# Performance work log

Hardware: AMD Instinct MI355X
Metric: run time of the kernel (lower is better)

## Reference

```python
import jax, jax.numpy as jnp
import numpy as np

T, H, W = 4, 16, 16
S = T * H * W          # 1024 flattened sequence length
C = 576                # embd_dim
NH = 8                 # n_head
DK = C // NH           # 72 per-head dim
L = 4                  # n_layer
B = 4                  # batch
PD = C // 3            # 192 per-axis pos-embed dim


def setup_inputs() -> dict:
    key = jax.random.key(0)
    ks = jax.random.split(key, 10)
    s = 1.0 / np.sqrt(C)
    return {
        "x": jax.random.normal(ks[0], (B, T, H, W, C), jnp.float32),
        "pos0": jax.random.normal(ks[1], (T, PD), jnp.float32) * 0.01,
        "pos1": jax.random.normal(ks[2], (H, PD), jnp.float32) * 0.01,
        "pos2": jax.random.normal(ks[3], (W, PD), jnp.float32) * 0.01,
        "ln1_g": jnp.ones((L, C), jnp.float32),
        "ln1_b": jnp.zeros((L, C), jnp.float32),
        "wq": jax.random.normal(ks[4], (L, C, C), jnp.float32) * s,
        "wk": jax.random.normal(ks[5], (L, C, C), jnp.float32) * s,
        "wv": jax.random.normal(ks[6], (L, C, C), jnp.float32) * s,
        "wo": jax.random.normal(ks[7], (L, C, C), jnp.float32) * (s / np.sqrt(L)),
        "wo_b": jnp.zeros((L, C), jnp.float32),
        "ln2_g": jnp.ones((L, C), jnp.float32),
        "ln2_b": jnp.zeros((L, C), jnp.float32),
        "w1": jax.random.normal(ks[8], (L, C, 4 * C), jnp.float32) * s,
        "b1": jnp.zeros((L, 4 * C), jnp.float32),
        "w2": jax.random.normal(ks[9], (L, 4 * C, C), jnp.float32) * (s / 2.0),
        "b2": jnp.zeros((L, C), jnp.float32),
    }


def _layernorm(x, g, b):
    # Faithful to the source: float32 math, and (1e-5 + rsqrt(var)) multiplier
    # (note: source adds eps to rsqrt, not to var -- replicated exactly).
    xf = x.astype(jnp.float32)
    mu = xf.mean(-1, keepdims=True)
    var = jnp.mean(jnp.square(xf - mu), -1, keepdims=True)
    y = (xf - mu) * (1e-5 + jax.lax.rsqrt(var)) * g + b
    return y.astype(x.dtype)


def _stack(x, pos0, pos1, pos2, ln1_g, ln1_b, wq, wk, wv, wo, wo_b,
           ln2_g, ln2_b, w1, b1, w2, b2):
    b = x.shape[0]
    xf = x.reshape(b, S, C)
    # right_shift (decode_step=None): shift flattened tokens right by one
    xf = jnp.pad(xf[:, :-1], ((0, 0), (1, 0), (0, 0)))
    # broadcast positional embedding, concat along channel
    pos = jnp.concatenate([
        jnp.broadcast_to(pos0[:, None, None, :], (T, H, W, PD)),
        jnp.broadcast_to(pos1[None, :, None, :], (T, H, W, PD)),
        jnp.broadcast_to(pos2[None, None, :, :], (T, H, W, PD)),
    ], axis=-1).reshape(S, C)
    xf = xf + pos

    causal = jnp.tril(jnp.ones((S, S), bool))
    scale = 1.0 / np.sqrt(DK)
    neg_inf = jnp.float32(-jnp.inf)

    for l in range(L):  # fixed small layer loop
        # --- causal full self-attention ---
        h = _layernorm(xf, ln1_g[l], ln1_b[l])
        q = (h @ wq[l]).reshape(b, S, NH, DK).transpose(0, 2, 1, 3)
        k = (h @ wk[l]).reshape(b, S, NH, DK).transpose(0, 2, 1, 3)
        v = (h @ wv[l]).reshape(b, S, NH, DK).transpose(0, 2, 1, 3)
        att = jnp.einsum('bhqd,bhkd->bhqk', q, k) * scale
        att = jnp.where(causal, att, neg_inf)
        att = jax.nn.softmax(att, axis=-1)
        a = jnp.einsum('bhqk,bhkd->bhqd', att, v)
        a = a.transpose(0, 2, 1, 3).reshape(b, S, C)
        xf = xf + a @ wo[l] + wo_b[l]
        # --- FFN with GeLU2: sigmoid(1.702*x)*x ---
        h = _layernorm(xf, ln2_g[l], ln2_b[l])
        h = h @ w1[l] + b1[l]
        h = jax.nn.sigmoid(1.702 * h) * h
        xf = xf + h @ w2[l] + b2[l]
    return xf.reshape(b, T, H, W, C)


def reference(x, pos0, pos1, pos2, ln1_g, ln1_b, wq, wk, wv, wo, wo_b,
              ln2_g, ln2_b, w1, b1, w2, b2):
    return _stack(x, pos0, pos1, pos2, ln1_g, ln1_b, wq, wk, wv, wo, wo_b,
                  ln2_g, ln2_b, w1, b1, w2, b2)
```

## Files before the change

kernel.cpp:

```cpp
#include <hip/hip_runtime.h>
#include <hip/hip_bf16.h>

typedef __hip_bfloat16 bf16;
using bf16x8 = __attribute__((ext_vector_type(8))) short;
using f32x4  = __attribute__((ext_vector_type(4))) float;

#define S_LEN 1024
#define CDIM  576
#define NHEAD 8
#define DKH   72
#define BATCH 4
#define MROWS 4096
#define FFDIM 2304
#define QKVN  1728

__device__ __forceinline__ void gload16(const void* g, void* l) {
  __builtin_amdgcn_global_load_lds(
      (const __attribute__((address_space(1))) unsigned int*)g,
      (__attribute__((address_space(3))) unsigned int*)l, 16, 0, 0);
}

template <int N> __device__ __forceinline__ void wait_vmcnt() {
  if constexpr (N == 0)      asm volatile("s_waitcnt vmcnt(0)" ::: "memory");
  else if constexpr (N == 2) asm volatile("s_waitcnt vmcnt(2)" ::: "memory");
  else if constexpr (N == 3) asm volatile("s_waitcnt vmcnt(3)" ::: "memory");
  else if constexpr (N == 4) asm volatile("s_waitcnt vmcnt(4)" ::: "memory");
  else if constexpr (N == 6) asm volatile("s_waitcnt vmcnt(6)" ::: "memory");
}

__device__ __forceinline__ short f2bf_bits(float x) {
  unsigned int u = __float_as_uint(x);
  u += 0x7fffu + ((u >> 16) & 1u);
  return (short)(u >> 16);
}

__global__ __launch_bounds__(256) void transpose_cvt(
    const float* __restrict__ in, bf16* __restrict__ out, int K, int N,
    size_t in_ls, size_t out_ls) {
  __shared__ float tile[32][33];
  const float* inl = in + (size_t)blockIdx.z * in_ls;
  bf16* outl = out + (size_t)blockIdx.z * out_ls;
  int n0 = blockIdx.x * 32, k0 = blockIdx.y * 32;
  int tx = threadIdx.x & 31, ty = threadIdx.x >> 5;
#pragma unroll
  for (int i = 0; i < 32; i += 8)
    tile[ty + i][tx] = inl[(size_t)(k0 + ty + i) * N + (n0 + tx)];
  __syncthreads();
#pragma unroll
  for (int i = 0; i < 32; i += 8)
    outl[(size_t)(n0 + ty + i) * K + (k0 + tx)] = __float2bfloat16(tile[tx][ty + i]);
}

__global__ __launch_bounds__(256) void build_xf(
    const float* __restrict__ x, const float* __restrict__ p0,
    const float* __restrict__ p1, const float* __restrict__ p2,
    float* __restrict__ xf) {
  int idx = blockIdx.x * 256 + threadIdx.x;
  int c4 = idx % 144;
  int s  = (idx / 144) & (S_LEN - 1);
  int b  = idx / (144 * S_LEN);
  int c  = c4 * 4;
  int t = s >> 8, hh = (s >> 4) & 15, w = s & 15;
  float4 pv;
  if (c < 192)       pv = *(const float4*)&p0[t  * 192 + c];
  else if (c < 384)  pv = *(const float4*)&p1[hh * 192 + c - 192];
  else               pv = *(const float4*)&p2[w  * 192 + c - 384];
  float4 xv = make_float4(0.f, 0.f, 0.f, 0.f);
  if (s > 0) xv = *(const float4*)&x[((size_t)b * S_LEN + s - 1) * CDIM + c];
  float4 r = make_float4(xv.x + pv.x, xv.y + pv.y, xv.z + pv.z, xv.w + pv.w);
  *(float4*)&xf[((size_t)b * S_LEN + s) * CDIM + c] = r;
}

__global__ __launch_bounds__(256) void ln_kernel(
    const float* __restrict__ x, const float* __restrict__ g,
    const float* __restrict__ b, bf16* __restrict__ out) {
  int row  = blockIdx.x * 4 + (threadIdx.x >> 6);
  int lane = threadIdx.x & 63;
  const float* xr = x + (size_t)row * CDIM;
  float vals[9];
  float sum = 0.f;
#pragma unroll
  for (int i = 0; i < 9; i++) { vals[i] = xr[lane + 64 * i]; sum += vals[i]; }
#pragma unroll
  for (int o = 1; o < 64; o <<= 1) sum += __shfl_xor(sum, o);
  float mu = sum * (1.f / CDIM);
  float vs = 0.f;
#pragma unroll
  for (int i = 0; i < 9; i++) { float d = vals[i] - mu; vs += d * d; }
#pragma unroll
  for (int o = 1; o < 64; o <<= 1) vs += __shfl_xor(vs, o);
  float mult = 1e-5f + rsqrtf(vs * (1.f / CDIM));
  bf16* orow = out + (size_t)row * CDIM;
#pragma unroll
  for (int i = 0; i < 9; i++) {
    int c = lane + 64 * i;
    orow[c] = __float2bfloat16((vals[i] - mu) * mult * g[c] + b[c]);
  }
}

template <int BM, int BN, bool BIAS, bool RES, int ACT, bool OUTBF>
__global__ __launch_bounds__(256) void gemm3(
    const bf16* __restrict__ A, const bf16* __restrict__ Bt,
    const float* __restrict__ bias, const float* __restrict__ res,
    void* __restrict__ outp, int N, int K) {
  constexpr int MI = BM / 32;
  constexpr int NI = BN / 32;
  constexpr int AJ = BM / 64;
  constexpr int BJ = BN / 64;
  constexpr int LPS = AJ + BJ;
  __shared__ __align__(16) short ldsA[4][BM * 32];
  __shared__ __align__(16) short ldsB[4][BN * 32];
  const int tid = threadIdx.x, lane = tid & 63, wave = tid >> 6;
  const int lr = lane & 15, quad = lane >> 4;
  const int m0 = blockIdx.x * BM, n0 = blockIdx.y * BN;
  const int wm = (wave & 1) * (BM / 2), wn = (wave >> 1) * (BN / 2);
  f32x4 acc[MI][NI] = {};

  const int srow = lane >> 2, scol = (lane & 3) * 8;
  const short* Ag[AJ];
  int ldsAo[AJ];
#pragma unroll
  for (int j = 0; j < AJ; j++) {
    Ag[j] = (const short*)A + (size_t)(m0 + (wave * AJ + j) * 16 + srow) * K + scol;
    ldsAo[j] = (wave * AJ + j) * 512;
  }
  const short* Bg[BJ];
  int ldsBo[BJ];
#pragma unroll
  for (int j = 0; j < BJ; j++) {
    Bg[j] = (const short*)Bt + (size_t)(n0 + (wave * BJ + j) * 16 + srow) * K + scol;
    ldsBo[j] = (wave * BJ + j) * 512;
  }

#pragma unroll
  for (int j = 0; j < AJ; j++) gload16(Ag[j], &ldsA[0][ldsAo[j]]);
#pragma unroll
  for (int j = 0; j < BJ; j++) gload16(Bg[j], &ldsB[0][ldsBo[j]]);
#pragma unroll
  for (int j = 0; j < AJ; j++) gload16(Ag[j] + 32, &ldsA[1][ldsAo[j]]);
#pragma unroll
  for (int j = 0; j < BJ; j++) gload16(Bg[j] + 32, &ldsB[1][ldsBo[j]]);

  int bi = 0;
  for (int k0 = 0; k0 < K; k0 += 32, bi = (bi + 1) & 3) {
    if (k0 + 64 < K) {
      const int sb = (bi + 2) & 3;
#pragma unroll
      for (int j = 0; j < AJ; j++) gload16(Ag[j] + k0 + 64, &ldsA[sb][ldsAo[j]]);
#pragma unroll
      for (int j = 0; j < BJ; j++) gload16(Bg[j] + k0 + 64, &ldsB[sb][ldsBo[j]]);
      wait_vmcnt<2 * LPS>();
    } else if (k0 + 32 < K) {
      wait_vmcnt<LPS>();
    } else {
      wait_vmcnt<0>();
    }
    __builtin_amdgcn_s_barrier();
    __builtin_amdgcn_sched_barrier(0);
    bf16x8 af[MI], bfv[NI];
#pragma unroll
    for (int mi = 0; mi < MI; mi++)
      af[mi] = *(const bf16x8*)&ldsA[bi][(wm + mi * 16 + lr) * 32 + quad * 8];
#pragma unroll
    for (int ni = 0; ni < NI; ni++)
      bfv[ni] = *(const bf16x8*)&ldsB[bi][(wn + ni * 16 + lr) * 32 + quad * 8];
#pragma unroll
    for (int mi = 0; mi < MI; mi++)
#pragma unroll
      for (int ni = 0; ni < NI; ni++)
        acc[mi][ni] = __builtin_amdgcn_mfma_f32_16x16x32_bf16(af[mi], bfv[ni], acc[mi][ni], 0, 0, 0);
  }

  float* fout = (float*)outp;
  bf16*  bout = (bf16*)outp;
#pragma unroll
  for (int mi = 0; mi < MI; mi++)
#pragma unroll
    for (int ni = 0; ni < NI; ni++) {
      int col = n0 + wn + ni * 16 + lr;
#pragma unroll
      for (int r = 0; r < 4; r++) {
        int row = m0 + wm + mi * 16 + quad * 4 + r;
        float v = acc[mi][ni][r];
        if (BIAS) v += bias[col];
        if (ACT == 1) v = v / (1.f + __expf(-1.702f * v));
        size_t idx = (size_t)row * N + col;
        if (RES) v += res[idx];
        if (OUTBF) bout[idx] = __float2bfloat16(v);
        else       fout[idx] = v;
      }
    }
}

__global__ __launch_bounds__(256) void attn_mfma(
    const bf16* __restrict__ qkv, bf16* __restrict__ a) {
  __shared__ __align__(16) short ldsK[2][9 * 512];
  __shared__ __align__(16) short ldsVt[2][80][104];
  __shared__ __align__(16) short ldsP[4 * 1024];
  const int bh = blockIdx.y, b = bh >> 3, h = bh & 7;
  const int tid = threadIdx.x, wave = tid >> 6, lane = tid & 63;
  const int lr = lane & 15, quad = lane >> 4;
  const int qt = (blockIdx.y < 16) ? (15 - (int)blockIdx.x) : (int)blockIdx.x;
  const float scale = 0.11785113019775793f;
  const int qcol = h * DKH, kcol = CDIM + h * DKH, vcol = 2 * CDIM + h * DKH;

  const int qrow = qt * 64 + wave * 16 + lr;
  const short* qg = (const short*)qkv + (size_t)(b * S_LEN + qrow) * QKVN + qcol;
  bf16x8 qfrag[3];
#pragma unroll
  for (int c = 0; c < 3; c++) {
    int d0 = c * 32 + quad * 8;
    bf16x8 z = {0, 0, 0, 0, 0, 0, 0, 0};
    qfrag[c] = (d0 < DKH) ? *(const bf16x8*)(qg + d0) : z;
  }
  f32x4 oacc[5] = {};
  float m[4], l[4];
#pragma unroll
  for (int r = 0; r < 4; r++) { m[r] = -1e30f; l[r] = 0.f; }

  const size_t ktstep = (size_t)64 * QKVN;
  const short* kg0 = (const short*)qkv + (size_t)(b * S_LEN + wave * 16 + lr) * QKVN + kcol + quad * 8;
  const short* kg2 = (const short*)qkv + (size_t)(b * S_LEN + lane) * QKVN + kcol + 64;
  const int vkey = tid & 63, vdgb = tid >> 6;
  const short* vg0 = (const short*)qkv + (size_t)(b * S_LEN + vkey) * QKVN + vcol;

  {
#pragma unroll
    for (int c = 0; c < 2; c++)
      gload16(kg0 + c * 32, &ldsK[0][(wave * 2 + c) * 512]);
    if (wave == 0) gload16(kg2, &ldsK[0][8 * 512]);
#pragma unroll
    for (int pass = 0; pass < 3; pass++) {
      int d0 = (vdgb + pass * 4) * 8;
      if (d0 < 80) {
        bf16x8 vv = {0, 0, 0, 0, 0, 0, 0, 0};
        if (d0 < DKH) vv = *(const bf16x8*)(vg0 + d0);
#pragma unroll
        for (int j = 0; j < 8; j++) ldsVt[0][d0 + j][vkey] = vv[j];
      }
    }
  }
  __syncthreads();

  for (int kt = 0; kt <= qt; kt++) {
    const int cur = kt & 1, nxt = cur ^ 1;
    const bool pf = (kt < qt);
    bf16x8 vpre[3];
    if (pf) {
      const short* kg = kg0 + (size_t)(kt + 1) * ktstep;
#pragma unroll
      for (int c = 0; c < 2; c++)
        gload16(kg + c * 32, &ldsK[nxt][(wave * 2 + c) * 512]);
      if (wave == 0) gload16(kg2 + (size_t)(kt + 1) * ktstep, &ldsK[nxt][8 * 512]);
      const short* vg = vg0 + (size_t)(kt + 1) * ktstep;
#pragma unroll
      for (int pass = 0; pass < 3; pass++) {
        int d0 = (vdgb + pass * 4) * 8;
        bf16x8 z = {0, 0, 0, 0, 0, 0, 0, 0};
        vpre[pass] = (d0 < DKH) ? *(const bf16x8*)(vg + d0) : z;
      }
    }
    f32x4 sacc[4] = {};
    __builtin_amdgcn_s_setprio(1);
#pragma unroll
    for (int nc = 0; nc < 4; nc++) {
      bf16x8 kf0 = *(const bf16x8*)&ldsK[cur][(nc * 2 + 0) * 512 + lane * 8];
      sacc[nc] = __builtin_amdgcn_mfma_f32_16x16x32_bf16(qfrag[0], kf0, sacc[nc], 0, 0, 0);
      bf16x8 kf1 = *(const bf16x8*)&ldsK[cur][(nc * 2 + 1) * 512 + lane * 8];
      sacc[nc] = __builtin_amdgcn_mfma_f32_16x16x32_bf16(qfrag[1], kf1, sacc[nc], 0, 0, 0);
      bf16x8 kf2 = *(const bf16x8*)&ldsK[cur][8 * 512 + (nc * 16 + lr) * 8];
      sacc[nc] = __builtin_amdgcn_mfma_f32_16x16x32_bf16(qfrag[2], kf2, sacc[nc], 0, 0, 0);
    }
    __builtin_amdgcn_s_setprio(0);
    float pmax[4];
#pragma unroll
    for (int r = 0; r < 4; r++) pmax[r] = -1e30f;
    bool diag = (kt == qt);
#pragma unroll
    for (int nc = 0; nc < 4; nc++)
#pragma unroll
      for (int r = 0; r < 4; r++) {
        float s = sacc[nc][r] * scale;
        if (diag && (nc * 16 + lr > wave * 16 + quad * 4 + r)) s = -1e30f;
        sacc[nc][r] = s;
        pmax[r] = fmaxf(pmax[r], s);
      }
    bool within = (pmax[0] - m[0] <= 8.f) && (pmax[1] - m[1] <= 8.f) &&
                  (pmax[2] - m[2] <= 8.f) && (pmax[3] - m[3] <= 8.f);
    if (!__all(within)) {
      float tmax[4];
#pragma unroll
      for (int r = 0; r < 4; r++) {
        tmax[r] = pmax[r];
        tmax[r] = fmaxf(tmax[r], __shfl_xor(tmax[r], 1));
        tmax[r] = fmaxf(tmax[r], __shfl_xor(tmax[r], 2));
        tmax[r] = fmaxf(tmax[r], __shfl_xor(tmax[r], 4));
        tmax[r] = fmaxf(tmax[r], __shfl_xor(tmax[r], 8));
      }
#pragma unroll
      for (int r = 0; r < 4; r++) {
        float mn = fmaxf(m[r], tmax[r]);
        float alpha = __expf(m[r] - mn);
        m[r] = mn;
        l[r] *= alpha;
#pragma unroll
        for (int dc = 0; dc < 5; dc++) oacc[dc][r] *= alpha;
      }
    }
    float psum[4];
#pragma unroll
    for (int r = 0; r < 4; r++) psum[r] = 0.f;
#pragma unroll
    for (int nc = 0; nc < 4; nc++)
#pragma unroll
      for (int r = 0; r < 4; r++) {
        float p = __expf(sacc[nc][r] - m[r]);
        psum[r] += p;
        int col = nc * 16 + lr;
        ldsP[wave * 1024 + (col >> 5) * 512 +
             (((col >> 3) & 3) * 16 + quad * 4 + r) * 8 + (col & 7)] = f2bf_bits(p);
      }
    bf16x8 pfrag[2];
#pragma unroll
    for (int kc = 0; kc < 2; kc++)
      pfrag[kc] = *(const bf16x8*)&ldsP[wave * 1024 + kc * 512 + lane * 8];
    __builtin_amdgcn_s_setprio(1);
#pragma unroll
    for (int dc = 0; dc < 5; dc++)
#pragma unroll
      for (int kc = 0; kc < 2; kc++) {
        bf16x8 vf = *(const bf16x8*)&ldsVt[cur][dc * 16 + lr][kc * 32 + quad * 8];
        oacc[dc] = __builtin_amdgcn_mfma_f32_16x16x32_bf16(pfrag[kc], vf, oacc[dc], 0, 0, 0);
      }
    __builtin_amdgcn_s_setprio(0);
#pragma unroll
    for (int r = 0; r < 4; r++) {
      psum[r] += __shfl_xor(psum[r], 1);
      psum[r] += __shfl_xor(psum[r], 2);
      psum[r] += __shfl_xor(psum[r], 4);
      psum[r] += __shfl_xor(psum[r], 8);
      l[r] += psum[r];
    }
    if (pf) {
#pragma unroll
      for (int pass = 0; pass < 3; pass++) {
        int d0 = (vdgb + pass * 4) * 8;
        if (d0 < 80) {
#pragma unroll
          for (int j = 0; j < 8; j++) ldsVt[nxt][d0 + j][vkey] = vpre[pass][j];
        }
      }
    }
    __syncthreads();
  }

#pragma unroll
  for (int dc = 0; dc < 5; dc++) {
    int d = dc * 16 + lr;
    if (d < DKH) {
#pragma unroll
      for (int r = 0; r < 4; r++) {
        int row = qt * 64 + wave * 16 + quad * 4 + r;
        float val = oacc[dc][r] / l[r];
        a[(size_t)(b * S_LEN + row) * CDIM + h * DKH + d] = __float2bfloat16(val);
      }
    }
  }
}

extern "C" void kernel_launch(void* const* d_in, const int* in_sizes, int n_in,
                              void* d_out, int out_size, void* d_ws, size_t ws_size,
                              hipStream_t stream) {
  const float* x    = (const float*)d_in[0];
  const float* pos0 = (const float*)d_in[1];
  const float* pos1 = (const float*)d_in[2];
  const float* pos2 = (const float*)d_in[3];
  const float* ln1g = (const float*)d_in[4];
  const float* ln1b = (const float*)d_in[5];
  const float* wq   = (const float*)d_in[6];
  const float* wk   = (const float*)d_in[7];
  const float* wv   = (const float*)d_in[8];
  const float* wo   = (const float*)d_in[9];
  const float* wob  = (const float*)d_in[10];
  const float* ln2g = (const float*)d_in[11];
  const float* ln2b = (const float*)d_in[12];
  const float* w1   = (const float*)d_in[13];
  const float* b1   = (const float*)d_in[14];
  const float* w2   = (const float*)d_in[15];
  const float* b2   = (const float*)d_in[16];

  char* ws = (char*)d_ws;
  size_t off = 0;
  auto alloc = [&](size_t bytes) {
    char* p = ws + off;
    off += (bytes + 255) & ~(size_t)255;
    return p;
  };
  bf16* wqkvT = (bf16*)alloc((size_t)4 * QKVN * CDIM * sizeof(bf16));
  bf16* woT   = (bf16*)alloc((size_t)4 * CDIM * CDIM * sizeof(bf16));
  bf16* w1T   = (bf16*)alloc((size_t)4 * FFDIM * CDIM * sizeof(bf16));
  bf16* w2T   = (bf16*)alloc((size_t)4 * CDIM * FFDIM * sizeof(bf16));
  bf16* hbuf  = (bf16*)alloc((size_t)MROWS * CDIM * sizeof(bf16));
  bf16* abuf  = (bf16*)alloc((size_t)MROWS * CDIM * sizeof(bf16));
  bf16* ubuf  = (bf16*)alloc((size_t)MROWS * FFDIM * sizeof(bf16));
  bf16* qkvb  = (bf16*)alloc((size_t)MROWS * QKVN * sizeof(bf16));
  float* xf   = (float*)d_out;

  const size_t ils  = (size_t)CDIM * CDIM;
  const size_t ils2 = (size_t)CDIM * FFDIM;
  const size_t qkv_ls = (size_t)QKVN * CDIM;
  transpose_cvt<<<dim3(18, 18, 4), 256, 0, stream>>>(wq, wqkvT, CDIM, CDIM, ils, qkv_ls);
  transpose_cvt<<<dim3(18, 18, 4), 256, 0, stream>>>(wk, wqkvT + (size_t)CDIM * CDIM, CDIM, CDIM, ils, qkv_ls);
  transpose_cvt<<<dim3(18, 18, 4), 256, 0, stream>>>(wv, wqkvT + (size_t)2 * CDIM * CDIM, CDIM, CDIM, ils, qkv_ls);
  transpose_cvt<<<dim3(18, 18, 4), 256, 0, stream>>>(wo, woT, CDIM, CDIM, ils, ils);
  transpose_cvt<<<dim3(72, 18, 4), 256, 0, stream>>>(w1, w1T, CDIM, FFDIM, ils2, ils2);
  transpose_cvt<<<dim3(18, 72, 4), 256, 0, stream>>>(w2, w2T, FFDIM, CDIM, ils2, ils2);

  build_xf<<<2304, 256, 0, stream>>>(x, pos0, pos1, pos2, xf);

  for (int l = 0; l < 4; l++) {
    bf16* wqkv_l = wqkvT + (size_t)l * qkv_ls;
    bf16* wo_l   = woT   + (size_t)l * ils;
    bf16* w1_l   = w1T   + (size_t)l * ils2;
    bf16* w2_l   = w2T   + (size_t)l * ils2;

    ln_kernel<<<1024, 256, 0, stream>>>(xf, ln1g + l * CDIM, ln1b + l * CDIM, hbuf);
    gemm3<128, 64, false, false, 0, true><<<dim3(32, QKVN / 64), 256, 0, stream>>>(
        hbuf, wqkv_l, nullptr, nullptr, qkvb, QKVN, CDIM);
    attn_mfma<<<dim3(16, 32), 256, 0, stream>>>(qkvb, abuf);
    gemm3<64, 64, true, true, 0, false><<<dim3(64, CDIM / 64), 256, 0, stream>>>(
        abuf, wo_l, wob + l * CDIM, xf, xf, CDIM, CDIM);
    ln_kernel<<<1024, 256, 0, stream>>>(xf, ln2g + l * CDIM, ln2b + l * CDIM, hbuf);
    gemm3<128, 64, true, false, 1, true><<<dim3(32, FFDIM / 64), 256, 0, stream>>>(
        hbuf, w1_l, b1 + l * FFDIM, nullptr, ubuf, FFDIM, CDIM);
    gemm3<64, 64, true, true, 0, false><<<dim3(64, CDIM / 64), 256, 0, stream>>>(
        ubuf, w2_l, b2 + l * CDIM, xf, xf, CDIM, FFDIM);
  }
}
```

Baseline: 681.0 us.

## Make each wave own an independent 64x64 GEMM tile without block barriers

After: 688.4 us. About the same (+1.1%).

```diff
diff --git a/kernel.cpp b/kernel.cpp
--- a/kernel.cpp
+++ b/kernel.cpp
@@ -22,10 +22,7 @@
 
 template <int N> __device__ __forceinline__ void wait_vmcnt() {
   if constexpr (N == 0)      asm volatile("s_waitcnt vmcnt(0)" ::: "memory");
-  else if constexpr (N == 2) asm volatile("s_waitcnt vmcnt(2)" ::: "memory");
-  else if constexpr (N == 3) asm volatile("s_waitcnt vmcnt(3)" ::: "memory");
-  else if constexpr (N == 4) asm volatile("s_waitcnt vmcnt(4)" ::: "memory");
-  else if constexpr (N == 6) asm volatile("s_waitcnt vmcnt(6)" ::: "memory");
+  else if constexpr (N == 8) asm volatile("s_waitcnt vmcnt(8)" ::: "memory");
 }
 
 __device__ __forceinline__ short f2bf_bits(float x) {
@@ -98,89 +95,72 @@
   }
 }
 
-template <int BM, int BN, bool BIAS, bool RES, int ACT, bool OUTBF>
-__global__ __launch_bounds__(256) void gemm3(
+template <bool BIAS, bool RES, int ACT, bool OUTBF>
+__global__ __launch_bounds__(256) void gemm4(
     const bf16* __restrict__ A, const bf16* __restrict__ Bt,
     const float* __restrict__ bias, const float* __restrict__ res,
     void* __restrict__ outp, int N, int K) {
-  constexpr int MI = BM / 32;
-  constexpr int NI = BN / 32;
-  constexpr int AJ = BM / 64;
-  constexpr int BJ = BN / 64;
-  constexpr int LPS = AJ + BJ;
-  __shared__ __align__(16) short ldsA[4][BM * 32];
-  __shared__ __align__(16) short ldsB[4][BN * 32];
+  __shared__ __align__(16) short lds[4][2][2][2048];
   const int tid = threadIdx.x, lane = tid & 63, wave = tid >> 6;
   const int lr = lane & 15, quad = lane >> 4;
-  const int m0 = blockIdx.x * BM, n0 = blockIdx.y * BN;
-  const int wm = (wave & 1) * (BM / 2), wn = (wave >> 1) * (BN / 2);
-  f32x4 acc[MI][NI] = {};
+  const int g = blockIdx.x * 4 + wave;
+  const int mt = g & 63, nt = g >> 6;
+  const int m0 = mt * 64, n0 = nt * 64;
+  f32x4 acc[4][4] = {};
 
   const int srow = lane >> 2, scol = (lane & 3) * 8;
-  const short* Ag[AJ];
-  int ldsAo[AJ];
-#pragma unroll
-  for (int j = 0; j < AJ; j++) {
-    Ag[j] = (const short*)A + (size_t)(m0 + (wave * AJ + j) * 16 + srow) * K + scol;
-    ldsAo[j] = (wave * AJ + j) * 512;
-  }
-  const short* Bg[BJ];
-  int ldsBo[BJ];
-#pragma unroll
-  for (int j = 0; j < BJ; j++) {
-    Bg[j] = (const short*)Bt + (size_t)(n0 + (wave * BJ + j) * 16 + srow) * K + scol;
-    ldsBo[j] = (wave * BJ + j) * 512;
-  }
-
-#pragma unroll
-  for (int j = 0; j < AJ; j++) gload16(Ag[j], &ldsA[0][ldsAo[j]]);
-#pragma unroll
-  for (int j = 0; j < BJ; j++) gload16(Bg[j], &ldsB[0][ldsBo[j]]);
-#pragma unroll
-  for (int j = 0; j < AJ; j++) gload16(Ag[j] + 32, &ldsA[1][ldsAo[j]]);
-#pragma unroll
-  for (int j = 0; j < BJ; j++) gload16(Bg[j] + 32, &ldsB[1][ldsBo[j]]);
-
-  int bi = 0;
-  for (int k0 = 0; k0 < K; k0 += 32, bi = (bi + 1) & 3) {
-    if (k0 + 64 < K) {
-      const int sb = (bi + 2) & 3;
-#pragma unroll
-      for (int j = 0; j < AJ; j++) gload16(Ag[j] + k0 + 64, &ldsA[sb][ldsAo[j]]);
-#pragma unroll
-      for (int j = 0; j < BJ; j++) gload16(Bg[j] + k0 + 64, &ldsB[sb][ldsBo[j]]);
-      wait_vmcnt<2 * LPS>();
-    } else if (k0 + 32 < K) {
-      wait_vmcnt<LPS>();
+  const short* Ag[4];
+  const short* Bg[4];
+#pragma unroll
+  for (int j = 0; j < 4; j++) {
+    Ag[j] = (const short*)A  + (size_t)(m0 + j * 16 + srow) * K + scol;
+    Bg[j] = (const short*)Bt + (size_t)(n0 + j * 16 + srow) * K + scol;
+  }
+
+  const int T = K / 32;
+#pragma unroll
+  for (int j = 0; j < 4; j++) gload16(Ag[j], &lds[wave][0][0][j * 512]);
+#pragma unroll
+  for (int j = 0; j < 4; j++) gload16(Bg[j], &lds[wave][0][1][j * 512]);
+
+  int cur = 0;
+  for (int t = 0; t < T; ++t, cur ^= 1) {
+    if (t + 1 < T) {
+      const int nxt = cur ^ 1, k1 = (t + 1) * 32;
+#pragma unroll
+      for (int j = 0; j < 4; j++) gload16(Ag[j] + k1, &lds[wave][nxt][0][j * 512]);
+#pragma unroll
+      for (int j = 0; j < 4; j++) gload16(Bg[j] + k1, &lds[wave][nxt][1][j * 512]);
+      wait_vmcnt<8>();
     } else {
       wait_vmcnt<0>();
     }
-    __builtin_amdgcn_s_barrier();
     __builtin_amdgcn_sched_barrier(0);
-    bf16x8 af[MI], bfv[NI];
-#pragma unroll
-    for (int mi = 0; mi < MI; mi++)
-      af[mi] = *(const bf16x8*)&ldsA[bi][(wm + mi * 16 + lr) * 32 + quad * 8];
-#pragma unroll
-    for (int ni = 0; ni < NI; ni++)
-      bfv[ni] = *(const bf16x8*)&ldsB[bi][(wn + ni * 16 + lr) * 32 + quad * 8];
-#pragma unroll
-    for (int mi = 0; mi < MI; mi++)
-#pragma unroll
-      for (int ni = 0; ni < NI; ni++)
+    bf16x8 af[4], bfv[4];
+#pragma unroll
+    for (int mi = 0; mi < 4; mi++)
+      af[mi] = *(const bf16x8*)&lds[wave][cur][0][(mi * 16 + lr) * 32 + quad * 8];
+#pragma unroll
+    for (int ni = 0; ni < 4; ni++)
+      bfv[ni] = *(const bf16x8*)&lds[wave][cur][1][(ni * 16 + lr) * 32 + quad * 8];
+#pragma unroll
+    for (int mi = 0; mi < 4; mi++)
+#pragma unroll
+      for (int ni = 0; ni < 4; ni++)
         acc[mi][ni] = __builtin_amdgcn_mfma_f32_16x16x32_bf16(af[mi], bfv[ni], acc[mi][ni], 0, 0, 0);
+    __builtin_amdgcn_sched_barrier(0);
   }
 
   float* fout = (float*)outp;
   bf16*  bout = (bf16*)outp;
 #pragma unroll
-  for (int mi = 0; mi < MI; mi++)
-#pragma unroll
-    for (int ni = 0; ni < NI; ni++) {
-      int col = n0 + wn + ni * 16 + lr;
-#pragma unroll
-      for (int r = 0; r < 4; r++) {
-        int row = m0 + wm + mi * 16 + quad * 4 + r;
+  for (int mi = 0; mi < 4; mi++)
+#pragma unroll
+    for (int ni = 0; ni < 4; ni++) {
+      int col = n0 + ni * 16 + lr;
+#pragma unroll
+      for (int r = 0; r < 4; r++) {
+        int row = m0 + mi * 16 + quad * 4 + r;
         float v = acc[mi][ni][r];
         if (BIAS) v += bias[col];
         if (ACT == 1) v = v / (1.f + __expf(-1.702f * v));
@@ -425,15 +405,15 @@
     bf16* w2_l   = w2T   + (size_t)l * ils2;
 
     ln_kernel<<<1024, 256, 0, stream>>>(xf, ln1g + l * CDIM, ln1b + l * CDIM, hbuf);
-    gemm3<128, 64, false, false, 0, true><<<dim3(32, QKVN / 64), 256, 0, stream>>>(
+    gemm4<false, false, 0, true><<<dim3(64 * (QKVN / 64) / 4), 256, 0, stream>>>(
         hbuf, wqkv_l, nullptr, nullptr, qkvb, QKVN, CDIM);
     attn_mfma<<<dim3(16, 32), 256, 0, stream>>>(qkvb, abuf);
-    gemm3<64, 64, true, true, 0, false><<<dim3(64, CDIM / 64), 256, 0, stream>>>(
+    gemm4<true, true, 0, false><<<dim3(64 * (CDIM / 64) / 4), 256, 0, stream>>>(
         abuf, wo_l, wob + l * CDIM, xf, xf, CDIM, CDIM);
     ln_kernel<<<1024, 256, 0, stream>>>(xf, ln2g + l * CDIM, ln2b + l * CDIM, hbuf);
-    gemm3<128, 64, true, false, 1, true><<<dim3(32, FFDIM / 64), 256, 0, stream>>>(
+    gemm4<true, false, 1, true><<<dim3(64 * (FFDIM / 64) / 4), 256, 0, stream>>>(
         hbuf, w1_l, b1 + l * FFDIM, nullptr, ubuf, FFDIM, CDIM);
-    gemm3<64, 64, true, true, 0, false><<<dim3(64, CDIM / 64), 256, 0, stream>>>(
+    gemm4<true, true, 0, false><<<dim3(64 * (CDIM / 64) / 4), 256, 0, stream>>>(
         ubuf, w2_l, b2 + l * CDIM, xf, xf, CDIM, FFDIM);
   }
 }
```
